# Kernel optimization log

Hardware: AMD Instinct MI355X
Metric: run time of the kernel (lower is better)

The kernel has to match this reference:

```python
import jax, jax.numpy as jnp
import numpy as np

D = 1024      # in/out token dims
E = 2048      # expanded dim = 2*D
S_ATT = 128   # attention feature dim s
EPS = 1e-5
SQRT_S = np.sqrt(S_ATT).astype(np.float32)


def setup_inputs() -> dict:
    key = jax.random.key(0)
    ks = jax.random.split(key, 8)
    B, S = 4, 2048
    x = jax.random.normal(ks[0], (B, S, D), dtype=jnp.float32)
    pos_enc = jax.random.normal(ks[1], (S, S_ATT), dtype=jnp.float32)
    # uv Linear: xavier_uniform on weight of shape [2e+s, D]
    fan_out = 2 * E + S_ATT
    limit = np.sqrt(6.0 / (D + fan_out)).astype(np.float32)
    uv_w = jax.random.uniform(ks[2], (fan_out, D), dtype=jnp.float32, minval=-limit, maxval=limit)
    # o Linear: default kaiming-uniform-ish; plain uniform works for a reference
    lim_o = np.sqrt(1.0 / E).astype(np.float32)
    o_w = jax.random.uniform(ks[3], (D, E), dtype=jnp.float32, minval=-lim_o, maxval=lim_o)
    gamma = jax.random.uniform(ks[4], (2, S_ATT), dtype=jnp.float32)
    beta = jax.random.uniform(ks[5], (2, S_ATT), dtype=jnp.float32)
    ln_g = jnp.ones((), dtype=jnp.float32)          # ScaleNorm learnable scalar
    res_scale = jnp.ones((D,), dtype=jnp.float32)   # ChannelWiseScale
    return {"x": x, "pos_enc": pos_enc, "uv_w": uv_w, "o_w": o_w,
            "gamma": gamma, "beta": beta, "ln_g": ln_g, "res_scale": res_scale}


def _gau(x, pos_enc, uv_w, o_w, gamma, beta, ln_g, res_scale):
    # ScaleNorm: x / max(||x|| * d^-0.5, eps) * g
    norm = jnp.linalg.norm(x, axis=-1, keepdims=True) * (D ** -0.5)
    xn = x / jnp.maximum(norm, EPS) * ln_g
    uv = jax.nn.silu(jnp.einsum('bsd,fd->bsf', xn, uv_w))  # [B,S,2E+s]
    u, v, base = uv[..., :E], uv[..., E:2 * E], uv[..., 2 * E:]
    # per-head affine: base[...,None,:]*gamma+beta -> q,k
    qk_base = base[..., None, :] * gamma + beta             # [B,S,2,s]
    q = qk_base[..., 0, :] + pos_enc[None, :, :]            # 'add' pos enc
    k = qk_base[..., 1, :] + pos_enc[None, :, :]
    scores = jnp.einsum('bqs,bks->bqk', q, k) / SQRT_S
    kernel = jnp.square(jax.nn.relu(scores))                # squared-ReLU attention
    attn_v = jnp.einsum('bqk,bke->bqe', kernel, v)
    out = jnp.einsum('bqe,de->bqd', u * attn_v, o_w)
    # residual shortcut with channel-wise scale (in == out dims)
    return x * res_scale + out


def reference(x, pos_enc, uv_w, o_w, gamma, beta, ln_g, res_scale):
    return _gau(x, pos_enc, uv_w, o_w, gamma, beta, ln_g, res_scale)
```

## Files before the change

### kernel.cpp

```cpp
#include <hip/hip_runtime.h>

typedef unsigned short u16;
typedef __bf16 bf16x8 __attribute__((ext_vector_type(8)));
typedef float f32x4 __attribute__((ext_vector_type(4)));

#define SEQ   2048
#define DDIM  1024
#define EDIM  2048
#define FDIM  4224
#define SATT  128
#define NBATCH 4

__device__ __forceinline__ u16 f2bf(float f) {
  unsigned u = __float_as_uint(f);
  unsigned r = (u + 0x7fffu + ((u >> 16) & 1u)) >> 16;
  return (u16)r;
}
__device__ __forceinline__ float bf2f(u16 v) {
  return __uint_as_float(((unsigned)v) << 16);
}

__device__ __forceinline__ void gload16(const u16* g, u16* l) {
  auto gp = (const __attribute__((address_space(1))) u16*)(unsigned long long)g;
  auto lp = (__attribute__((address_space(3))) u16*)(unsigned)(unsigned long long)l;
  __builtin_amdgcn_global_load_lds(gp, lp, 16, 0, 0);
}


__global__ void cvt_bf16_kernel(const float* __restrict__ in, u16* __restrict__ out, int n4) {
  int i = blockIdx.x * blockDim.x + threadIdx.x;
  if (i >= n4) return;
  float4 v = reinterpret_cast<const float4*>(in)[i];
  unsigned p0 = (unsigned)f2bf(v.x) | ((unsigned)f2bf(v.y) << 16);
  unsigned p1 = (unsigned)f2bf(v.z) | ((unsigned)f2bf(v.w) << 16);
  uint2 pk; pk.x = p0; pk.y = p1;
  reinterpret_cast<uint2*>(out)[i] = pk;
}

__global__ void rms_kernel(const float* __restrict__ x, const float* __restrict__ ln_g,
                           u16* __restrict__ xn) {
  int row = blockIdx.x;
  int t = threadIdx.x;
  const float4* xr = reinterpret_cast<const float4*>(x + (size_t)row * DDIM);
  float4 v = xr[t];
  float s = v.x * v.x + v.y * v.y + v.z * v.z + v.w * v.w;
#pragma unroll
  for (int off = 32; off > 0; off >>= 1) s += __shfl_down(s, off);
  __shared__ float wsum[4];
  int lane = t & 63, wv = t >> 6;
  if (lane == 0) wsum[wv] = s;
  __syncthreads();
  float tot = wsum[0] + wsum[1] + wsum[2] + wsum[3];
  float rms = sqrtf(tot * (1.0f / (float)DDIM));
  float scale = ln_g[0] / fmaxf(rms, 1e-5f);
  unsigned p0 = (unsigned)f2bf(v.x * scale) | ((unsigned)f2bf(v.y * scale) << 16);
  unsigned p1 = (unsigned)f2bf(v.z * scale) | ((unsigned)f2bf(v.w * scale) << 16);
  uint2 pk; pk.x = p0; pk.y = p1;
  reinterpret_cast<uint2*>(xn + (size_t)row * DDIM)[t] = pk;
}

__global__ void qk_kernel(const u16* __restrict__ uv, const float* __restrict__ pos_enc,
                          const float* __restrict__ gamma, const float* __restrict__ beta,
                          u16* __restrict__ q, u16* __restrict__ k) {
  int r = blockIdx.x;
  int t = threadIdx.x;
  int s = r & (SEQ - 1);
  float bval = bf2f(uv[(size_t)r * FDIM + 2 * EDIM + t]);
  float pe = pos_enc[(size_t)s * SATT + t];
  float qv = bval * gamma[t] + beta[t] + pe;
  float kv = bval * gamma[SATT + t] + beta[SATT + t] + pe;
  q[(size_t)r * SATT + t] = f2bf(qv);
  k[(size_t)r * SATT + t] = f2bf(kv);
}

__global__ void transpose_v(const u16* __restrict__ uv, u16* __restrict__ vt) {
  __shared__ u16 tile[32][33];
  int b = blockIdx.z;
  uv += (size_t)b * SEQ * FDIM;
  vt += (size_t)b * EDIM * SEQ;
  int e0 = blockIdx.x * 32, s0 = blockIdx.y * 32;
  int tx = threadIdx.x, ty = threadIdx.y;
#pragma unroll
  for (int j = 0; j < 32; j += 8)
    tile[ty + j][tx] = uv[(size_t)(s0 + ty + j) * FDIM + EDIM + e0 + tx];
  __syncthreads();
#pragma unroll
  for (int j = 0; j < 32; j += 8)
    vt[(size_t)(e0 + ty + j) * SEQ + s0 + tx] = tile[tx][ty + j];
}

template <int EPI>
__global__ __launch_bounds__(512, 2) void gemm_bt2(
    const u16* __restrict__ A, const u16* __restrict__ B,
    int M, int N, int K,
    u16* __restrict__ Cbf, float* __restrict__ Cf,
    const u16* __restrict__ U, int ldu,
    const float* __restrict__ Xres, const float* __restrict__ rscale,
    size_t sA, size_t sB, size_t sC, size_t sU) {
  __shared__ u16 lds[3 * 24576];
  const int tid = threadIdx.x;
  const int w = tid >> 6, l = tid & 63;
  const int wr = w >> 1, wc = w & 1;
  const int fr = l & 15, kg = l >> 4;

  const int bz = blockIdx.z;
  A += (size_t)bz * sA; B += (size_t)bz * sB; U += (size_t)bz * sU;

  const int nbx = gridDim.x;
  int li = blockIdx.y * nbx + blockIdx.x;
  const int cpx = (nbx * gridDim.y) >> 3;
  li = (li & 7) * cpx + (li >> 3);
  const int bn = li % nbx;
  const int bm = li / nbx;

  const int NT = K >> 6;
  const int srow = (w << 3) + (l >> 3);
  const int scol = (((l & 7) ^ (l >> 3)) & 7) << 3;
  const size_t aoff = (size_t)bm * 256 * K;
  const size_t boff = (size_t)bn * 128 * K;
  const char* ldsC = (const char*)lds;

  auto stageAu = [&](int t, int h) {
    int sb = (t % 3) * 24576 + h * 8192;
    const u16* g = A + aoff + (size_t)(h * 128 + srow) * K + t * 64 + scol;
#pragma unroll
    for (int L = 0; L < 2; L++)
      gload16(g + (size_t)(L * 64) * K, &lds[sb + (L * 8 + w) * 512]);
  };
  auto stageBu = [&](int t) {
    int sb = (t % 3) * 24576 + 16384;
    const u16* g = B + boff + (size_t)srow * K + t * 64 + scol;
#pragma unroll
    for (int L = 0; L < 2; L++)
      gload16(g + (size_t)(L * 64) * K, &lds[sb + (L * 8 + w) * 512]);
  };
  auto ldA = [&](int cur, int i, int s) -> bf16x8 {
    int r = ((wr & 1) << 6) + (i << 4) + fr;
    int off = cur * 49152 + ((wr >> 1) << 14) + (r << 7) + (s << 6) + (kg << 4);
    off ^= (r & 7) << 4;
    return *(const bf16x8*)(ldsC + off);
  };
  auto ldB = [&](int cur, int j, int s) -> bf16x8 {
    int r = (wc << 6) + (j << 4) + fr;
    int off = cur * 49152 + 32768 + (r << 7) + (s << 6) + (kg << 4);
    off ^= (r & 7) << 4;
    return *(const bf16x8*)(ldsC + off);
  };

  f32x4 acc[4][4];
#pragma unroll
  for (int i = 0; i < 4; i++)
#pragma unroll
    for (int j = 0; j < 4; j++) acc[i][j] = f32x4{0.f, 0.f, 0.f, 0.f};

  stageAu(0, 0); stageAu(0, 1); stageBu(0);
  if (NT > 1) { stageAu(1, 0); stageAu(1, 1); stageBu(1); }
  asm volatile("s_waitcnt vmcnt(6)" ::: "memory");
  __builtin_amdgcn_s_barrier();

  bf16x8 aF[2][2], bF[2][2][2];
  for (int t = 0; t < NT; ++t) {
    const int cur = t % 3;
    const bool st = (t + 2 < NT);
#pragma unroll
    for (int i = 0; i < 2; i++)
#pragma unroll
      for (int s = 0; s < 2; s++) aF[i][s] = ldA(cur, i, s);
#pragma unroll
    for (int j = 0; j < 2; j++)
#pragma unroll
      for (int s = 0; s < 2; s++) bF[0][j][s] = ldB(cur, j, s);
    if (st) stageAu(t + 2, 0);
    __builtin_amdgcn_s_barrier();
    __builtin_amdgcn_s_setprio(1);
#pragma unroll
    for (int s = 0; s < 2; s++)
#pragma unroll
      for (int i = 0; i < 2; i++)
#pragma unroll
        for (int j = 0; j < 2; j++)
          acc[i][j] = __builtin_amdgcn_mfma_f32_16x16x32_bf16(aF[i][s], bF[0][j][s], acc[i][j], 0, 0, 0);
    __builtin_amdgcn_s_setprio(0);
    __builtin_amdgcn_s_barrier();
#pragma unroll
    for (int j = 0; j < 2; j++)
#pragma unroll
      for (int s = 0; s < 2; s++) bF[1][j][s] = ldB(cur, 2 + j, s);
    if (st) stageAu(t + 2, 1);
    __builtin_amdgcn_s_barrier();
    __builtin_amdgcn_s_setprio(1);
#pragma unroll
    for (int s = 0; s < 2; s++)
#pragma unroll
      for (int i = 0; i < 2; i++)
#pragma unroll
        for (int j = 0; j < 2; j++)
          acc[i][2 + j] = __builtin_amdgcn_mfma_f32_16x16x32_bf16(aF[i][s], bF[1][j][s], acc[i][2 + j], 0, 0, 0);
    __builtin_amdgcn_s_setprio(0);
    __builtin_amdgcn_s_barrier();
#pragma unroll
    for (int i = 0; i < 2; i++)
#pragma unroll
      for (int s = 0; s < 2; s++) aF[i][s] = ldA(cur, 2 + i, s);
    if (st) stageBu(t + 2);
    __builtin_amdgcn_s_barrier();
    __builtin_amdgcn_s_setprio(1);
#pragma unroll
    for (int s = 0; s < 2; s++)
#pragma unroll
      for (int i = 0; i < 2; i++)
#pragma unroll
        for (int j = 0; j < 2; j++)
          acc[2 + i][j] = __builtin_amdgcn_mfma_f32_16x16x32_bf16(aF[i][s], bF[0][j][s], acc[2 + i][j], 0, 0, 0);
    __builtin_amdgcn_s_setprio(0);
    __builtin_amdgcn_s_barrier();
    __builtin_amdgcn_s_setprio(1);
#pragma unroll
    for (int s = 0; s < 2; s++)
#pragma unroll
      for (int i = 0; i < 2; i++)
#pragma unroll
        for (int j = 0; j < 2; j++)
          acc[2 + i][2 + j] = __builtin_amdgcn_mfma_f32_16x16x32_bf16(aF[i][s], bF[1][j][s], acc[2 + i][2 + j], 0, 0, 0);
    __builtin_amdgcn_s_setprio(0);
    if (st) asm volatile("s_waitcnt vmcnt(6)" ::: "memory");
    else    asm volatile("s_waitcnt vmcnt(0)" ::: "memory");
    __builtin_amdgcn_s_barrier();
  }

  const int m0 = bm * 256 + wr * 64;
  const int n0 = bn * 128 + wc * 64;
  const int rsub = (l >> 4) * 4;
  const int ccol = l & 15;
#pragma unroll
  for (int i = 0; i < 4; i++) {
#pragma unroll
    for (int j = 0; j < 4; j++) {
      int n = n0 + j * 16 + ccol;
#pragma unroll
      for (int tt = 0; tt < 4; tt++) {
        int m = m0 + i * 16 + rsub + tt;
        float v = acc[i][j][tt];
        size_t idx = (size_t)m * N + n;
        if constexpr (EPI == 0) {
          float sv = v / (1.f + __expf(-v));
          Cbf[(size_t)bz * sC + idx] = f2bf(sv);
        } else if constexpr (EPI == 1) {
          float sc = v * 0.08838834764831845f;
          sc = sc > 0.f ? sc * sc : 0.f;
          Cbf[(size_t)bz * sC + idx] = f2bf(sc);
        } else if constexpr (EPI == 2) {
          float uvl = bf2f(U[(size_t)m * ldu + n]);
          Cbf[(size_t)bz * sC + idx] = f2bf(v * uvl);
        } else {
          Cf[idx] = Xres[idx] * rscale[n] + v;
        }
      }
    }
  }
}

template <int EPI>
__global__ __launch_bounds__(256) void gemm_bt(
    const u16* __restrict__ A, const u16* __restrict__ B,
    int M, int N, int K,
    u16* __restrict__ Cbf, float* __restrict__ Cf,
    const u16* __restrict__ U, int ldu,
    const float* __restrict__ Xres, const float* __restrict__ rscale,
    size_t sA, size_t sB, size_t sC, size_t sU) {
  __shared__ u16 As[128 * 32];
  __shared__ u16 Bs[128 * 32];
  const int tid = threadIdx.x;
  const int wave = tid >> 6, lane = tid & 63;
  const int wr = wave >> 1, wc = wave & 1;
  const int bz = blockIdx.z;
  A += (size_t)bz * sA; B += (size_t)bz * sB; U += (size_t)bz * sU;
  const int nbx = gridDim.x;
  int li = blockIdx.y * nbx + blockIdx.x;
  const int cpx = (nbx * gridDim.y) >> 3;
  li = (li & 7) * cpx + (li >> 3);
  const int bn = li % nbx;
  const int bm = li / nbx;
  const size_t abase = (size_t)bm * 128 * K;
  const size_t bbase = (size_t)bn * 128 * K;
  const int srow = tid >> 2;
  const int scol = (tid & 3) * 8;
  f32x4 acc[4][4];
#pragma unroll
  for (int i = 0; i < 4; i++)
#pragma unroll
    for (int j = 0; j < 4; j++) acc[i][j] = f32x4{0.f, 0.f, 0.f, 0.f};
  const int fr = lane & 15;
  const int fk = (lane >> 4) * 8;
  for (int k0 = 0; k0 < K; k0 += 32) {
#pragma unroll
    for (int r = 0; r < 2; r++) {
      const u16* gA = A + abase + (size_t)(r * 64 + srow) * K + k0 + scol;
      const u16* gB = B + bbase + (size_t)(r * 64 + srow) * K + k0 + scol;
      gload16(gA, As + r * 2048 + wave * 512);
      gload16(gB, Bs + r * 2048 + wave * 512);
    }
    __syncthreads();
    bf16x8 af[4], bfr[4];
#pragma unroll
    for (int i = 0; i < 4; i++) {
      af[i]  = *reinterpret_cast<const bf16x8*>(&As[(wr * 64 + i * 16 + fr) * 32 + fk]);
      bfr[i] = *reinterpret_cast<const bf16x8*>(&Bs[(wc * 64 + i * 16 + fr) * 32 + fk]);
    }
#pragma unroll
    for (int i = 0; i < 4; i++)
#pragma unroll
      for (int j = 0; j < 4; j++)
        acc[i][j] = __builtin_amdgcn_mfma_f32_16x16x32_bf16(af[i], bfr[j], acc[i][j], 0, 0, 0);
    __syncthreads();
  }
  const int m0 = bm * 128 + wr * 64;
  const int n0 = bn * 128 + wc * 64;
  const int rsub = (lane >> 4) * 4;
  const int ccol = lane & 15;
#pragma unroll
  for (int i = 0; i < 4; i++) {
#pragma unroll
    for (int j = 0; j < 4; j++) {
      int n = n0 + j * 16 + ccol;
#pragma unroll
      for (int t = 0; t < 4; t++) {
        int m = m0 + i * 16 + rsub + t;
        float v = acc[i][j][t];
        size_t idx = (size_t)m * N + n;
        if constexpr (EPI == 0) {
          float sv = v / (1.f + __expf(-v));
          Cbf[(size_t)bz * sC + idx] = f2bf(sv);
        } else if constexpr (EPI == 1) {
          float sc = v * 0.08838834764831845f;
          sc = sc > 0.f ? sc * sc : 0.f;
          Cbf[(size_t)bz * sC + idx] = f2bf(sc);
        } else if constexpr (EPI == 2) {
          float uvl = bf2f(U[(size_t)m * ldu + n]);
          Cbf[(size_t)bz * sC + idx] = f2bf(v * uvl);
        } else {
          Cf[idx] = Xres[idx] * rscale[n] + v;
        }
      }
    }
  }
}


extern "C" void kernel_launch(void* const* d_in, const int* in_sizes, int n_in,
                              void* d_out, int out_size, void* d_ws, size_t ws_size,
                              hipStream_t stream) {
  const float* x        = (const float*)d_in[0];
  const float* pos_enc  = (const float*)d_in[1];
  const float* uv_w     = (const float*)d_in[2];
  const float* o_w      = (const float*)d_in[3];
  const float* gamma    = (const float*)d_in[4];
  const float* beta     = (const float*)d_in[5];
  const float* ln_g     = (const float*)d_in[6];
  const float* res_scale= (const float*)d_in[7];
  float* out = (float*)d_out;

  const size_t SZ_UVW  = (size_t)FDIM * DDIM * 2;
  const size_t SZ_OW   = (size_t)DDIM * EDIM * 2;
  const size_t SZ_Z    = (size_t)NBATCH * SEQ * EDIM * 2;
  const size_t SZ_XN   = (size_t)NBATCH * SEQ * DDIM * 2;
  const size_t SZ_UV   = (size_t)NBATCH * SEQ * FDIM * 2;
  const size_t SZ_QK   = (size_t)NBATCH * SEQ * SATT * 2;
  const size_t SZ_VT1  = (size_t)EDIM * SEQ * 2;
  const size_t SZ_P1   = (size_t)SEQ * SEQ * 2;
  auto al = [](size_t b) { return (b + 255) & ~(size_t)255; };
  const size_t need_full =
      al(SZ_UVW) + al(SZ_OW) + al(SZ_Z) + al(SZ_XN) + al(SZ_UV) + 2 * al(SZ_QK) +
      (size_t)NBATCH * (al(SZ_VT1) + al(SZ_P1));
  const bool FULL = ws_size >= need_full;

  char* p = (char*)d_ws;
  auto alloc = [&](size_t bytes) {
    char* r = p;
    p += (bytes + 255) & ~(size_t)255;
    return r;
  };
  u16* uvw_bf = (u16*)alloc(SZ_UVW);
  u16* ow_bf  = (u16*)alloc(SZ_OW);
  u16* z      = (u16*)alloc(SZ_Z);
  u16* vt     = (u16*)alloc(FULL ? (size_t)NBATCH * al(SZ_VT1) : SZ_VT1);
  u16* pmat   = (u16*)alloc(FULL ? (size_t)NBATCH * al(SZ_P1) : SZ_P1);
  size_t fixed = (size_t)(p - (char*)d_ws);
  const size_t perbc = (size_t)SEQ * DDIM * 2 + (size_t)SEQ * FDIM * 2 +
                       2 * (size_t)SEQ * SATT * 2 + 4 * 256;
  int BC = FULL ? NBATCH : ((ws_size >= fixed + 4 * perbc) ? 4 : 1);
  u16* xn = (u16*)alloc((size_t)BC * SEQ * DDIM * 2);
  u16* uv = (u16*)alloc((size_t)BC * SEQ * FDIM * 2);
  u16* qb = (u16*)alloc((size_t)BC * SEQ * SATT * 2);
  u16* kb = (u16*)alloc((size_t)BC * SEQ * SATT * 2);

  const size_t sVT = (al(SZ_VT1) >> 1);
  const size_t sP  = (al(SZ_P1) >> 1);

  {
    int n4 = FDIM * DDIM / 4;
    cvt_bf16_kernel<<<(n4 + 255) / 256, 256, 0, stream>>>(uv_w, uvw_bf, n4);
    n4 = DDIM * EDIM / 4;
    cvt_bf16_kernel<<<(n4 + 255) / 256, 256, 0, stream>>>(o_w, ow_bf, n4);
  }

  if (FULL) {
    const int rows = NBATCH * SEQ;
    rms_kernel<<<rows, 256, 0, stream>>>(x, ln_g, xn);
    gemm_bt2<0><<<dim3(FDIM / 128, rows / 256), 512, 0, stream>>>(
        xn, uvw_bf, rows, FDIM, DDIM, uv, nullptr, nullptr, 0, nullptr, nullptr,
        0, 0, 0, 0);
    qk_kernel<<<rows, SATT, 0, stream>>>(uv, pos_enc, gamma, beta, qb, kb);
    transpose_v<<<dim3(EDIM / 32, SEQ / 32, NBATCH), dim3(32, 8), 0, stream>>>(uv, vt);
    gemm_bt2<1><<<dim3(SEQ / 128, SEQ / 256, NBATCH), 512, 0, stream>>>(
        qb, kb, SEQ, SEQ, SATT, pmat, nullptr, nullptr, 0, nullptr, nullptr,
        (size_t)SEQ * SATT, (size_t)SEQ * SATT, sP, 0);
    gemm_bt2<2><<<dim3(EDIM / 128, SEQ / 256, NBATCH), 512, 0, stream>>>(
        pmat, vt, SEQ, EDIM, SEQ, z, nullptr, uv, FDIM, nullptr, nullptr,
        sP, sVT, (size_t)SEQ * EDIM, (size_t)SEQ * FDIM);
    gemm_bt2<3><<<dim3(DDIM / 128, rows / 256), 512, 0, stream>>>(
        z, ow_bf, rows, DDIM, EDIM, nullptr, out, nullptr, 0,
        x, res_scale, 0, 0, 0, 0);
  } else {
    for (int b0 = 0; b0 < NBATCH; b0 += BC) {
      int rows = BC * SEQ;
      rms_kernel<<<rows, 256, 0, stream>>>(x + (size_t)b0 * SEQ * DDIM, ln_g, xn);
      gemm_bt<0><<<dim3(FDIM / 128, rows / 128), 256, 0, stream>>>(
          xn, uvw_bf, rows, FDIM, DDIM, uv, nullptr, nullptr, 0, nullptr, nullptr,
          0, 0, 0, 0);
      qk_kernel<<<rows, SATT, 0, stream>>>(uv, pos_enc, gamma, beta, qb, kb);
      for (int bb = 0; bb < BC; bb++) {
        int b = b0 + bb;
        const u16* uvb = uv + (size_t)bb * SEQ * FDIM;
        transpose_v<<<dim3(EDIM / 32, SEQ / 32, 1), dim3(32, 8), 0, stream>>>(uvb, vt);
        gemm_bt<1><<<dim3(SEQ / 128, SEQ / 128), 256, 0, stream>>>(
            qb + (size_t)bb * SEQ * SATT, kb + (size_t)bb * SEQ * SATT,
            SEQ, SEQ, SATT, pmat, nullptr, nullptr, 0, nullptr, nullptr,
            0, 0, 0, 0);
        gemm_bt<2><<<dim3(EDIM / 128, SEQ / 128), 256, 0, stream>>>(
            pmat, vt, SEQ, EDIM, SEQ, z + (size_t)b * SEQ * EDIM, nullptr,
            uvb, FDIM, nullptr, nullptr, 0, 0, 0, 0);
      }
    }
    gemm_bt<3><<<dim3(DDIM / 128, (NBATCH * SEQ) / 128), 256, 0, stream>>>(
        z, ow_bf, NBATCH * SEQ, DDIM, EDIM, nullptr, out, nullptr, 0,
        x, res_scale, 0, 0, 0, 0);
  }
}
```

Measured before the change: 316.7 us.

## Add 256x256-tile ping-pong GEMM kernel and pad uv width for the first three GEMMs

Adds a new gemm_bt3 kernel that computes 256x256 output tiles with 8 waves. It double-buffers 64 KB LDS stages split into quarter-tile loads, interleaved with MFMA phases under s_setprio. The kernel is used for the uv projection, the scores GEMM and the attention-V GEMM. The uv width is padded from 4224 to 4352 so it divides into 256-wide tiles, with the padded weight rows zeroed by memset. The larger tiles aim to raise arithmetic intensity and overlap loads with math, at the cost of a larger padded uv buffer, extra wasted columns, and fewer blocks for the small scores GEMM.

```diff
diff --git a/kernel.cpp b/kernel.cpp
--- a/kernel.cpp
+++ b/kernel.cpp
@@ -8,6 +8,7 @@
 #define DDIM  1024
 #define EDIM  2048
 #define FDIM  4224
+#define FPAD  4352
 #define SATT  128
 #define NBATCH 4
 
@@ -61,11 +62,11 @@
 
 __global__ void qk_kernel(const u16* __restrict__ uv, const float* __restrict__ pos_enc,
                           const float* __restrict__ gamma, const float* __restrict__ beta,
-                          u16* __restrict__ q, u16* __restrict__ k) {
+                          u16* __restrict__ q, u16* __restrict__ k, int ldF) {
   int r = blockIdx.x;
   int t = threadIdx.x;
   int s = r & (SEQ - 1);
-  float bval = bf2f(uv[(size_t)r * FDIM + 2 * EDIM + t]);
+  float bval = bf2f(uv[(size_t)r * ldF + 2 * EDIM + t]);
   float pe = pos_enc[(size_t)s * SATT + t];
   float qv = bval * gamma[t] + beta[t] + pe;
   float kv = bval * gamma[SATT + t] + beta[SATT + t] + pe;
@@ -73,20 +74,191 @@
   k[(size_t)r * SATT + t] = f2bf(kv);
 }
 
-__global__ void transpose_v(const u16* __restrict__ uv, u16* __restrict__ vt) {
+__global__ void transpose_v(const u16* __restrict__ uv, u16* __restrict__ vt, int ldF) {
   __shared__ u16 tile[32][33];
   int b = blockIdx.z;
-  uv += (size_t)b * SEQ * FDIM;
+  uv += (size_t)b * SEQ * ldF;
   vt += (size_t)b * EDIM * SEQ;
   int e0 = blockIdx.x * 32, s0 = blockIdx.y * 32;
   int tx = threadIdx.x, ty = threadIdx.y;
 #pragma unroll
   for (int j = 0; j < 32; j += 8)
-    tile[ty + j][tx] = uv[(size_t)(s0 + ty + j) * FDIM + EDIM + e0 + tx];
+    tile[ty + j][tx] = uv[(size_t)(s0 + ty + j) * ldF + EDIM + e0 + tx];
   __syncthreads();
 #pragma unroll
   for (int j = 0; j < 32; j += 8)
     vt[(size_t)(e0 + ty + j) * SEQ + s0 + tx] = tile[tx][ty + j];
+}
+
+template <int EPI>
+__global__ __launch_bounds__(512, 2) void gemm_bt3(
+    const u16* __restrict__ A, const u16* __restrict__ B,
+    int N, int K,
+    u16* __restrict__ Cbf,
+    const u16* __restrict__ U, int ldu,
+    size_t sA, size_t sB, size_t sC, size_t sU) {
+  __shared__ u16 lds[65536];
+  const int tid = threadIdx.x;
+  const int w = tid >> 6, l = tid & 63;
+  const int wm2 = w >> 2, wn2 = w & 3;
+  const int fr = l & 15, kg = l >> 4;
+
+  const int bz = blockIdx.z;
+  A += (size_t)bz * sA; B += (size_t)bz * sB; U += (size_t)bz * sU;
+
+  const int nbx = gridDim.x;
+  int li = blockIdx.y * nbx + blockIdx.x;
+  const int cpx = (nbx * gridDim.y) >> 3;
+  li = (li & 7) * cpx + (li >> 3);
+  const int bn = li % nbx;
+  const int bm = li / nbx;
+
+  const int NT = K >> 6;
+  const size_t aoff = (size_t)bm * 256 * K;
+  const size_t boff = (size_t)bn * 256 * K;
+
+  const int r0 = (w << 3) + (l >> 3);
+  const int cswz = (((l & 7) ^ (l >> 3)) & 7) << 3;
+
+  auto stageP = [&](int T, int p) {
+    int off = (T & 1) * 65536 + p * 16384;
+    const u16* g;
+    if (p == 0)      g = A + aoff;
+    else if (p == 1) g = A + aoff + (size_t)128 * K;
+    else if (p == 2) g = B + boff;
+    else             g = B + boff + (size_t)128 * K;
+    g += (size_t)r0 * K + (size_t)T * 64 + cswz;
+    u16* dst = lds + (off >> 1) + w * 512;
+    gload16(g, dst);
+    gload16(g + (size_t)64 * K, dst + 4096);
+  };
+
+  const char* ldsC = (const char*)lds;
+  auto ldA = [&](int buf, int qa, int i, int s) -> bf16x8 {
+    int row = wm2 * 64 + i * 16 + fr;
+    int off = buf * 65536 + qa * 16384 + row * 128 + s * 64 + kg * 16;
+    off ^= (fr & 7) << 4;
+    return *(const bf16x8*)(ldsC + off);
+  };
+  auto ldB = [&](int buf, int qb, int j, int s) -> bf16x8 {
+    int row = wn2 * 32 + j * 16 + fr;
+    int off = buf * 65536 + 32768 + qb * 16384 + row * 128 + s * 64 + kg * 16;
+    off ^= (fr & 7) << 4;
+    return *(const bf16x8*)(ldsC + off);
+  };
+
+  f32x4 acc[8][4];
+#pragma unroll
+  for (int i = 0; i < 8; i++)
+#pragma unroll
+    for (int j = 0; j < 4; j++) acc[i][j] = f32x4{0.f, 0.f, 0.f, 0.f};
+
+  stageP(0, 0); stageP(0, 2); stageP(0, 3); stageP(0, 1);
+  asm volatile("s_waitcnt vmcnt(0)" ::: "memory");
+  __builtin_amdgcn_s_barrier();
+
+  bf16x8 aH[4][2], bF[2][2][2];
+  for (int t = 0; t < NT; ++t) {
+    const int buf = t & 1;
+    const bool st = (t + 1 < NT);
+    asm volatile("s_waitcnt vmcnt(4)" ::: "memory");
+#pragma unroll
+    for (int i = 0; i < 4; i++)
+#pragma unroll
+      for (int s = 0; s < 2; s++) aH[i][s] = ldA(buf, 0, i, s);
+#pragma unroll
+    for (int j = 0; j < 2; j++)
+#pragma unroll
+      for (int s = 0; s < 2; s++) bF[0][j][s] = ldB(buf, 0, j, s);
+    if (st) stageP(t + 1, 0);
+    __builtin_amdgcn_s_barrier();
+    asm volatile("s_waitcnt lgkmcnt(0)" ::: "memory");
+    __builtin_amdgcn_s_setprio(1);
+#pragma unroll
+    for (int s = 0; s < 2; s++)
+#pragma unroll
+      for (int i = 0; i < 4; i++)
+#pragma unroll
+        for (int j = 0; j < 2; j++)
+          acc[i][j] = __builtin_amdgcn_mfma_f32_16x16x32_bf16(aH[i][s], bF[0][j][s], acc[i][j], 0, 0, 0);
+    __builtin_amdgcn_s_setprio(0);
+    __builtin_amdgcn_s_barrier();
+    asm volatile("s_waitcnt vmcnt(4)" ::: "memory");
+#pragma unroll
+    for (int j = 0; j < 2; j++)
+#pragma unroll
+      for (int s = 0; s < 2; s++) bF[1][j][s] = ldB(buf, 1, j, s);
+    if (st) stageP(t + 1, 2);
+    __builtin_amdgcn_s_barrier();
+    asm volatile("s_waitcnt lgkmcnt(0)" ::: "memory");
+    __builtin_amdgcn_s_setprio(1);
+#pragma unroll
+    for (int s = 0; s < 2; s++)
+#pragma unroll
+      for (int i = 0; i < 4; i++)
+#pragma unroll
+        for (int j = 0; j < 2; j++)
+          acc[i][2 + j] = __builtin_amdgcn_mfma_f32_16x16x32_bf16(aH[i][s], bF[1][j][s], acc[i][2 + j], 0, 0, 0);
+    __builtin_amdgcn_s_setprio(0);
+    __builtin_amdgcn_s_barrier();
+    asm volatile("s_waitcnt vmcnt(4)" ::: "memory");
+#pragma unroll
+    for (int i = 0; i < 4; i++)
+#pragma unroll
+      for (int s = 0; s < 2; s++) aH[i][s] = ldA(buf, 1, i, s);
+    if (st) stageP(t + 1, 3);
+    __builtin_amdgcn_s_barrier();
+    asm volatile("s_waitcnt lgkmcnt(0)" ::: "memory");
+    __builtin_amdgcn_s_setprio(1);
+#pragma unroll
+    for (int s = 0; s < 2; s++)
+#pragma unroll
+      for (int i = 0; i < 4; i++)
+#pragma unroll
+        for (int j = 0; j < 2; j++)
+          acc[4 + i][j] = __builtin_amdgcn_mfma_f32_16x16x32_bf16(aH[i][s], bF[0][j][s], acc[4 + i][j], 0, 0, 0);
+    __builtin_amdgcn_s_setprio(0);
+    __builtin_amdgcn_s_barrier();
+    if (st) stageP(t + 1, 1);
+    __builtin_amdgcn_s_barrier();
+    __builtin_amdgcn_s_setprio(1);
+#pragma unroll
+    for (int s = 0; s < 2; s++)
+#pragma unroll
+      for (int i = 0; i < 4; i++)
+#pragma unroll
+        for (int j = 0; j < 2; j++)
+          acc[4 + i][2 + j] = __builtin_amdgcn_mfma_f32_16x16x32_bf16(aH[i][s], bF[1][j][s], acc[4 + i][2 + j], 0, 0, 0);
+    __builtin_amdgcn_s_setprio(0);
+    __builtin_amdgcn_s_barrier();
+  }
+
+  const int rsub = (l >> 4) * 4;
+  const int ccol = l & 15;
+#pragma unroll
+  for (int ai = 0; ai < 8; ai++) {
+#pragma unroll
+    for (int bj = 0; bj < 4; bj++) {
+      int n = bn * 256 + (bj >> 1) * 128 + wn2 * 32 + (bj & 1) * 16 + ccol;
+#pragma unroll
+      for (int tt = 0; tt < 4; tt++) {
+        int m = bm * 256 + (ai >> 2) * 128 + wm2 * 64 + (ai & 3) * 16 + rsub + tt;
+        float v = acc[ai][bj][tt];
+        size_t idx = (size_t)m * N + n;
+        if constexpr (EPI == 0) {
+          float sv = v / (1.f + __expf(-v));
+          Cbf[(size_t)bz * sC + idx] = f2bf(sv);
+        } else if constexpr (EPI == 1) {
+          float sc = v * 0.08838834764831845f;
+          sc = sc > 0.f ? sc * sc : 0.f;
+          Cbf[(size_t)bz * sC + idx] = f2bf(sc);
+        } else {
+          float uvl = bf2f(U[(size_t)m * ldu + n]);
+          Cbf[(size_t)bz * sC + idx] = f2bf(v * uvl);
+        }
+      }
+    }
+  }
 }
 
 template <int EPI>
@@ -360,17 +532,17 @@
   const float* res_scale= (const float*)d_in[7];
   float* out = (float*)d_out;
 
-  const size_t SZ_UVW  = (size_t)FDIM * DDIM * 2;
+  auto al = [](size_t b) { return (b + 255) & ~(size_t)255; };
+  const size_t SZ_UVWP = (size_t)FPAD * DDIM * 2;
   const size_t SZ_OW   = (size_t)DDIM * EDIM * 2;
   const size_t SZ_Z    = (size_t)NBATCH * SEQ * EDIM * 2;
   const size_t SZ_XN   = (size_t)NBATCH * SEQ * DDIM * 2;
-  const size_t SZ_UV   = (size_t)NBATCH * SEQ * FDIM * 2;
+  const size_t SZ_UVP  = (size_t)NBATCH * SEQ * FPAD * 2;
   const size_t SZ_QK   = (size_t)NBATCH * SEQ * SATT * 2;
   const size_t SZ_VT1  = (size_t)EDIM * SEQ * 2;
   const size_t SZ_P1   = (size_t)SEQ * SEQ * 2;
-  auto al = [](size_t b) { return (b + 255) & ~(size_t)255; };
   const size_t need_full =
-      al(SZ_UVW) + al(SZ_OW) + al(SZ_Z) + al(SZ_XN) + al(SZ_UV) + 2 * al(SZ_QK) +
+      al(SZ_UVWP) + al(SZ_OW) + al(SZ_Z) + al(SZ_XN) + al(SZ_UVP) + 2 * al(SZ_QK) +
       (size_t)NBATCH * (al(SZ_VT1) + al(SZ_P1));
   const bool FULL = ws_size >= need_full;
 
@@ -380,70 +552,85 @@
     p += (bytes + 255) & ~(size_t)255;
     return r;
   };
-  u16* uvw_bf = (u16*)alloc(SZ_UVW);
+
+  if (FULL) {
+    u16* uvw_bf = (u16*)alloc(SZ_UVWP);
+    u16* ow_bf  = (u16*)alloc(SZ_OW);
+    u16* z      = (u16*)alloc(SZ_Z);
+    u16* vt     = (u16*)alloc((size_t)NBATCH * al(SZ_VT1));
+    u16* pmat   = (u16*)alloc((size_t)NBATCH * al(SZ_P1));
+    u16* xn     = (u16*)alloc(SZ_XN);
+    u16* uv     = (u16*)alloc(SZ_UVP);
+    u16* qb     = (u16*)alloc(SZ_QK);
+    u16* kb     = (u16*)alloc(SZ_QK);
+    const size_t sVT = al(SZ_VT1) >> 1;
+    const size_t sP  = al(SZ_P1) >> 1;
+    const int rows = NBATCH * SEQ;
+
+    hipMemsetAsync(uvw_bf + (size_t)FDIM * DDIM, 0,
+                   (size_t)(FPAD - FDIM) * DDIM * 2, stream);
+    cvt_bf16_kernel<<<(FDIM * DDIM / 4 + 255) / 256, 256, 0, stream>>>(
+        uv_w, uvw_bf, FDIM * DDIM / 4);
+    cvt_bf16_kernel<<<(DDIM * EDIM / 4 + 255) / 256, 256, 0, stream>>>(
+        o_w, ow_bf, DDIM * EDIM / 4);
+
+    rms_kernel<<<rows, 256, 0, stream>>>(x, ln_g, xn);
+    gemm_bt3<0><<<dim3(FPAD / 256, rows / 256), 512, 0, stream>>>(
+        xn, uvw_bf, FPAD, DDIM, uv, nullptr, 0, 0, 0, 0, 0);
+    qk_kernel<<<rows, SATT, 0, stream>>>(uv, pos_enc, gamma, beta, qb, kb, FPAD);
+    transpose_v<<<dim3(EDIM / 32, SEQ / 32, NBATCH), dim3(32, 8), 0, stream>>>(uv, vt, FPAD);
+    gemm_bt3<1><<<dim3(SEQ / 256, SEQ / 256, NBATCH), 512, 0, stream>>>(
+        qb, kb, SEQ, SATT, pmat, nullptr, 0,
+        (size_t)SEQ * SATT, (size_t)SEQ * SATT, sP, 0);
+    gemm_bt3<2><<<dim3(EDIM / 256, SEQ / 256, NBATCH), 512, 0, stream>>>(
+        pmat, vt, EDIM, SEQ, z, uv, FPAD,
+        sP, sVT, (size_t)SEQ * EDIM, (size_t)SEQ * FPAD);
+    gemm_bt2<3><<<dim3(DDIM / 128, rows / 256), 512, 0, stream>>>(
+        z, ow_bf, rows, DDIM, EDIM, nullptr, out, nullptr, 0,
+        x, res_scale, 0, 0, 0, 0);
+    return;
+  }
+
+  u16* uvw_bf = (u16*)alloc((size_t)FDIM * DDIM * 2);
   u16* ow_bf  = (u16*)alloc(SZ_OW);
   u16* z      = (u16*)alloc(SZ_Z);
-  u16* vt     = (u16*)alloc(FULL ? (size_t)NBATCH * al(SZ_VT1) : SZ_VT1);
-  u16* pmat   = (u16*)alloc(FULL ? (size_t)NBATCH * al(SZ_P1) : SZ_P1);
+  u16* vt     = (u16*)alloc(SZ_VT1);
+  u16* pmat   = (u16*)alloc(SZ_P1);
   size_t fixed = (size_t)(p - (char*)d_ws);
   const size_t perbc = (size_t)SEQ * DDIM * 2 + (size_t)SEQ * FDIM * 2 +
                        2 * (size_t)SEQ * SATT * 2 + 4 * 256;
-  int BC = FULL ? NBATCH : ((ws_size >= fixed + 4 * perbc) ? 4 : 1);
+  int BC = (ws_size >= fixed + 4 * perbc) ? 4 : 1;
   u16* xn = (u16*)alloc((size_t)BC * SEQ * DDIM * 2);
   u16* uv = (u16*)alloc((size_t)BC * SEQ * FDIM * 2);
   u16* qb = (u16*)alloc((size_t)BC * SEQ * SATT * 2);
   u16* kb = (u16*)alloc((size_t)BC * SEQ * SATT * 2);
 
-  const size_t sVT = (al(SZ_VT1) >> 1);
-  const size_t sP  = (al(SZ_P1) >> 1);
-
-  {
-    int n4 = FDIM * DDIM / 4;
-    cvt_bf16_kernel<<<(n4 + 255) / 256, 256, 0, stream>>>(uv_w, uvw_bf, n4);
-    n4 = DDIM * EDIM / 4;
-    cvt_bf16_kernel<<<(n4 + 255) / 256, 256, 0, stream>>>(o_w, ow_bf, n4);
-  }
-
-  if (FULL) {
-    const int rows = NBATCH * SEQ;
-    rms_kernel<<<rows, 256, 0, stream>>>(x, ln_g, xn);
-    gemm_bt2<0><<<dim3(FDIM / 128, rows / 256), 512, 0, stream>>>(
+  cvt_bf16_kernel<<<(FDIM * DDIM / 4 + 255) / 256, 256, 0, stream>>>(
+      uv_w, uvw_bf, FDIM * DDIM / 4);
+  cvt_bf16_kernel<<<(DDIM * EDIM / 4 + 255) / 256, 256, 0, stream>>>(
+      o_w, ow_bf, DDIM * EDIM / 4);
+
+  for (int b0 = 0; b0 < NBATCH; b0 += BC) {
+    int rows = BC * SEQ;
+    rms_kernel<<<rows, 256, 0, stream>>>(x + (size_t)b0 * SEQ * DDIM, ln_g, xn);
+    gemm_bt<0><<<dim3(FDIM / 128, rows / 128), 256, 0, stream>>>(
         xn, uvw_bf, rows, FDIM, DDIM, uv, nullptr, nullptr, 0, nullptr, nullptr,
         0, 0, 0, 0);
-    qk_kernel<<<rows, SATT, 0, stream>>>(uv, pos_enc, gamma, beta, qb, kb);
-    transpose_v<<<dim3(EDIM / 32, SEQ / 32, NBATCH), dim3(32, 8), 0, stream>>>(uv, vt);
-    gemm_bt2<1><<<dim3(SEQ / 128, SEQ / 256, NBATCH), 512, 0, stream>>>(
-        qb, kb, SEQ, SEQ, SATT, pmat, nullptr, nullptr, 0, nullptr, nullptr,
-        (size_t)SEQ * SATT, (size_t)SEQ * SATT, sP, 0);
-    gemm_bt2<2><<<dim3(EDIM / 128, SEQ / 256, NBATCH), 512, 0, stream>>>(
-        pmat, vt, SEQ, EDIM, SEQ, z, nullptr, uv, FDIM, nullptr, nullptr,
-        sP, sVT, (size_t)SEQ * EDIM, (size_t)SEQ * FDIM);
-    gemm_bt2<3><<<dim3(DDIM / 128, rows / 256), 512, 0, stream>>>(
-        z, ow_bf, rows, DDIM, EDIM, nullptr, out, nullptr, 0,
-        x, res_scale, 0, 0, 0, 0);
-  } else {
-    for (int b0 = 0; b0 < NBATCH; b0 += BC) {
-      int rows = BC * SEQ;
-      rms_kernel<<<rows, 256, 0, stream>>>(x + (size_t)b0 * SEQ * DDIM, ln_g, xn);
-      gemm_bt<0><<<dim3(FDIM / 128, rows / 128), 256, 0, stream>>>(
-          xn, uvw_bf, rows, FDIM, DDIM, uv, nullptr, nullptr, 0, nullptr, nullptr,
+    qk_kernel<<<rows, SATT, 0, stream>>>(uv, pos_enc, gamma, beta, qb, kb, FDIM);
+    for (int bb = 0; bb < BC; bb++) {
+      int b = b0 + bb;
+      const u16* uvb = uv + (size_t)bb * SEQ * FDIM;
+      transpose_v<<<dim3(EDIM / 32, SEQ / 32, 1), dim3(32, 8), 0, stream>>>(uvb, vt, FDIM);
+      gemm_bt<1><<<dim3(SEQ / 128, SEQ / 128), 256, 0, stream>>>(
+          qb + (size_t)bb * SEQ * SATT, kb + (size_t)bb * SEQ * SATT,
+          SEQ, SEQ, SATT, pmat, nullptr, nullptr, 0, nullptr, nullptr,
           0, 0, 0, 0);
-      qk_kernel<<<rows, SATT, 0, stream>>>(uv, pos_enc, gamma, beta, qb, kb);
-      for (int bb = 0; bb < BC; bb++) {
-        int b = b0 + bb;
-        const u16* uvb = uv + (size_t)bb * SEQ * FDIM;
-        transpose_v<<<dim3(EDIM / 32, SEQ / 32, 1), dim3(32, 8), 0, stream>>>(uvb, vt);
-        gemm_bt<1><<<dim3(SEQ / 128, SEQ / 128), 256, 0, stream>>>(
-            qb + (size_t)bb * SEQ * SATT, kb + (size_t)bb * SEQ * SATT,
-            SEQ, SEQ, SATT, pmat, nullptr, nullptr, 0, nullptr, nullptr,
-            0, 0, 0, 0);
-        gemm_bt<2><<<dim3(EDIM / 128, SEQ / 128), 256, 0, stream>>>(
-            pmat, vt, SEQ, EDIM, SEQ, z + (size_t)b * SEQ * EDIM, nullptr,
-            uvb, FDIM, nullptr, nullptr, 0, 0, 0, 0);
-      }
+      gemm_bt<2><<<dim3(EDIM / 128, SEQ / 128), 256, 0, stream>>>(
+          pmat, vt, SEQ, EDIM, SEQ, z + (size_t)b * SEQ * EDIM, nullptr,
+          uvb, FDIM, nullptr, nullptr, 0, 0, 0, 0);
     }
-    gemm_bt<3><<<dim3(DDIM / 128, (NBATCH * SEQ) / 128), 256, 0, stream>>>(
-        z, ow_bf, NBATCH * SEQ, DDIM, EDIM, nullptr, out, nullptr, 0,
-        x, res_scale, 0, 0, 0, 0);
-  }
-}
+  }
+  gemm_bt<3><<<dim3(DDIM / 128, (NBATCH * SEQ) / 128), 256, 0, stream>>>(
+      z, ow_bf, NBATCH * SEQ, DDIM, EDIM, nullptr, out, nullptr, 0,
+      x, res_scale, 0, 0, 0, 0);
+}
```

Result: faster. 298.3 us (-5.8%).
